# Performance work log

Hardware: AMD Instinct MI355X
Metric: run time of the kernel (lower is better)

Reference implementation:

```python
import jax, jax.numpy as jnp
import numpy as np

ALPHA = 2.0      # spikingjelly surrogate.ATan default alpha
TAU_LIF = 2.0    # LIFNode tau
V_TH = 1.0       # spike threshold (v_reset = 0.0, hard reset)


@jax.custom_vjp
def spike_fn(x):
    # Heaviside forward (spikingjelly: x >= 0 -> 1)
    return (x >= 0.0).astype(x.dtype)

def _spike_fwd(x):
    return spike_fn(x), x

def _spike_bwd(x, g):
    # ATan surrogate gradient: alpha/2 / (1 + (pi/2 * alpha * x)^2)
    return (g * (ALPHA / 2.0) / (1.0 + (jnp.pi / 2.0 * ALPHA * x) ** 2),)

spike_fn.defvjp(_spike_fwd, _spike_bwd)


def setup_inputs() -> dict:
    key = jax.random.key(0)
    ks = jax.random.split(key, 5)
    B, T, I, H, O = 256, 1000, 700, 64, 20
    x = jax.random.normal(ks[0], (B, T, I), dtype=jnp.float32)
    W_h = jax.random.normal(ks[1], (H, I), dtype=jnp.float32) / np.sqrt(I).astype(np.float32)
    b_h = jnp.zeros((H,), dtype=jnp.float32)
    W_r = jax.random.normal(ks[2], (O, H), dtype=jnp.float32) / np.sqrt(H).astype(np.float32)
    b_r = jnp.zeros((O,), dtype=jnp.float32)
    tau_m = jax.random.uniform(ks[3], (O,), dtype=jnp.float32, minval=0.0, maxval=4.0)
    return {"x": x, "W_h": W_h, "b_h": b_h, "W_r": W_r, "b_r": b_r, "tau_m": tau_m}


def reference(x, W_h, b_h, W_r, b_r, tau_m):
    B, T, I = x.shape
    H = W_h.shape[0]
    O = W_r.shape[0]
    # One big GEMM for all hidden input currents: [T, B, H]
    currents = jnp.einsum('bti,hi->tbh', x, W_h) + b_h
    beta = jax.nn.sigmoid(tau_m)  # readout leak [O]
    # original accumulates softmax only for t > 10
    mask = (jnp.arange(T) > 10).astype(x.dtype)

    def step(carry, inp):
        v, v_ro, acc = carry
        cur, m = inp
        # LIF charge (decay_input=True, v_reset=0): v += (cur - v)/tau
        v = v + (cur - v) / TAU_LIF
        s = spike_fn(v - V_TH)
        # hard reset to v_reset = 0
        v = v * (1.0 - s)
        # readout leaky integrator
        ro_in = s @ W_r.T + b_r                      # [B, O]
        v_ro = v_ro * beta + (1.0 - beta) * ro_in
        acc = acc + m * jax.nn.softmax(v_ro, axis=-1)
        return (v, v_ro, acc), None

    init = (jnp.zeros((B, H), x.dtype),
            jnp.zeros((B, O), x.dtype),
            jnp.zeros((B, O), x.dtype))
    (_, _, acc), _ = jax.lax.scan(step, init, (currents, mask))
    return acc
```

## Files before the change

kernel.cpp:

```cpp
#include <hip/hip_runtime.h>


typedef float  f32x4  __attribute__((ext_vector_type(4)));
typedef short  short8 __attribute__((ext_vector_type(8)));
typedef unsigned long long ull;

#define B_   256
#define T_   1000
#define K_   700
#define H_   64
#define O_   20
#define NKT  22
#define TC   10
#define NC   100
#define TCL  100
#define NCL  10
#define BIL  40

#define OFF_WFRAG  ((size_t)0)
#define OFF_CUR    ((size_t)262144)
#define OFF_MASK   ((size_t)65798144)

__global__ void wprep(const float* __restrict__ Wh, unsigned short* __restrict__ wfrag) {
    int e = blockIdx.x * 256 + threadIdx.x;
    int kt   = e >> 8;
    int rem  = e & 255;
    int nf   = rem >> 6;
    int lane = rem & 63;
    int h     = nf * 16 + (lane & 15);
    int kbase = kt * 32 + ((lane >> 4) & 3) * 8;
    unsigned short* dh = wfrag + (size_t)kt * 4096 + (nf * 64 + lane) * 8;
    unsigned short* dl = dh + 2048;
#pragma unroll
    for (int j = 0; j < 8; ++j) {
        int k = kbase + j;
        float v = (k < K_) ? Wh[(size_t)h * K_ + k] : 0.0f;
        unsigned u  = __builtin_bit_cast(unsigned, v);
        float    fh = __builtin_bit_cast(float, u & 0xffff0000u);
        float    r  = v - fh;
        dh[j] = (unsigned short)(u >> 16);
        dl[j] = (unsigned short)(__builtin_bit_cast(unsigned, r) >> 16);
    }
}

__device__ __forceinline__ void glds16(const void* src, void* lds) {
    __builtin_amdgcn_global_load_lds(
        (const __attribute__((address_space(1))) void*)src,
        (__attribute__((address_space(3))) void*)lds, 16, 0, 0);
}

__device__ __forceinline__ void splitpair(f32x4 p0, f32x4 p1, short8& hi, short8& lo) {
#pragma unroll
    for (int j = 0; j < 4; ++j) {
        {
            unsigned u  = __builtin_bit_cast(unsigned, p0[j]);
            float    fh = __builtin_bit_cast(float, u & 0xffff0000u);
            float    r  = p0[j] - fh;
            hi[j] = (short)(u >> 16);
            lo[j] = (short)(__builtin_bit_cast(unsigned, r) >> 16);
        }
        {
            unsigned u  = __builtin_bit_cast(unsigned, p1[j]);
            float    fh = __builtin_bit_cast(float, u & 0xffff0000u);
            float    r  = p1[j] - fh;
            hi[j + 4] = (short)(u >> 16);
            lo[j + 4] = (short)(__builtin_bit_cast(unsigned, r) >> 16);
        }
    }
}

__device__ __forceinline__ void stage_x32(const float* __restrict__ x, size_t row0,
                                          int kt, int lane, int wid, float* sbuf) {
#pragma unroll
    for (int j = 0; j < 4; ++j) {
        int c   = j * 256 + wid * 64 + lane;
        int row = c >> 3;
        int col = c & 7;
        int csw = (col ^ (row & 7)) << 4;
        int kbyte = kt * 128 + csw;
        if (kbyte + 16 > K_ * 4) kbyte = 0;
        const char* src = (const char*)(x + (row0 + row) * (size_t)K_) + kbyte;
        float* dst = sbuf + (size_t)(j * 256 + wid * 64) * 4;
        glds16(src, dst);
    }
}

__device__ __forceinline__ void stage_w32(const unsigned short* __restrict__ wfrag,
                                          int kt, int lane, int wid, unsigned short* sbuf) {
#pragma unroll
    for (int j = 0; j < 2; ++j) {
        int c = j * 256 + wid * 64 + lane;
        int l = c ^ ((c >> 4) & 7);
        const unsigned short* src = wfrag + (size_t)kt * 4096 + l * 8;
        unsigned short* dst = sbuf + (size_t)(j * 256 + wid * 64) * 8;
        glds16(src, dst);
    }
}

__device__ __forceinline__ void compute32(const float* sbx_, const unsigned short* sbw_,
                                          int lane, int wid, f32x4 (&acc)[2][4]) {
    const f32x4*  xb = (const f32x4*)sbx_;
    const short8* wb = (const short8*)sbw_;
    short8 ah[2], al[2];
    int v0 = (lane >> 4) * 2;
#pragma unroll
    for (int i = 0; i < 2; ++i) {
        int r  = wid * 32 + i * 16 + (lane & 15);
        int c0 = r * 8 + (v0 ^ (r & 7));
        int c1 = r * 8 + ((v0 + 1) ^ (r & 7));
        splitpair(xb[c0], xb[c1], ah[i], al[i]);
    }
#pragma unroll
    for (int n = 0; n < 4; ++n) {
        int lh = n * 64 + lane;
        int ph = lh ^ ((lh >> 4) & 7);
        short8 bhf = wb[ph];
        short8 blf = wb[ph + 256];
#pragma unroll
        for (int i = 0; i < 2; ++i) {
            acc[i][n] = __builtin_amdgcn_mfma_f32_16x16x32_bf16(ah[i], bhf, acc[i][n], 0, 0, 0);
            acc[i][n] = __builtin_amdgcn_mfma_f32_16x16x32_bf16(al[i], bhf, acc[i][n], 0, 0, 0);
            acc[i][n] = __builtin_amdgcn_mfma_f32_16x16x32_bf16(ah[i], blf, acc[i][n], 0, 0, 0);
        }
    }
}

__global__ __launch_bounds__(256, 2) void gemm_cur(const float* __restrict__ x,
                                                   const unsigned short* __restrict__ wfrag,
                                                   const float* __restrict__ b_h,
                                                   float* __restrict__ cur) {
    __shared__ float          sbx[3][4096];
    __shared__ unsigned short sbw[3][4096];
    int tid  = threadIdx.x;
    int lane = tid & 63;
    int wid  = tid >> 6;
    size_t row0 = (size_t)blockIdx.x * 128;

    float bh4[4];
#pragma unroll
    for (int n = 0; n < 4; ++n) bh4[n] = b_h[n * 16 + (lane & 15)];

    f32x4 acc[2][4];
#pragma unroll
    for (int i = 0; i < 2; ++i)
#pragma unroll
        for (int n = 0; n < 4; ++n) acc[i][n] = (f32x4){0.f, 0.f, 0.f, 0.f};

    stage_x32(x, row0, 0, lane, wid, sbx[0]);  stage_w32(wfrag, 0, lane, wid, sbw[0]);
    stage_x32(x, row0, 1, lane, wid, sbx[1]);  stage_w32(wfrag, 1, lane, wid, sbw[1]);
    stage_x32(x, row0, 2, lane, wid, sbx[2]);  stage_w32(wfrag, 2, lane, wid, sbw[2]);

#define GSTEP(T, N)                                                          \
    {                                                                        \
        asm volatile("s_waitcnt vmcnt(" #N ")" ::: "memory");                \
        __builtin_amdgcn_s_barrier();                                        \
        compute32(sbx[(T) % 3], sbw[(T) % 3], lane, wid, acc);               \
        asm volatile("s_waitcnt lgkmcnt(0)" ::: "memory");                   \
        __builtin_amdgcn_s_barrier();                                        \
        if ((T) + 3 < NKT) {                                                 \
            stage_x32(x, row0, (T) + 3, lane, wid, sbx[(T) % 3]);            \
            stage_w32(wfrag, (T) + 3, lane, wid, sbw[(T) % 3]);              \
        }                                                                    \
    }
    GSTEP(0, 12)  GSTEP(1, 12)  GSTEP(2, 12)  GSTEP(3, 12)  GSTEP(4, 12)
    GSTEP(5, 12)  GSTEP(6, 12)  GSTEP(7, 12)  GSTEP(8, 12)  GSTEP(9, 12)
    GSTEP(10, 12) GSTEP(11, 12) GSTEP(12, 12) GSTEP(13, 12) GSTEP(14, 12)
    GSTEP(15, 12) GSTEP(16, 12) GSTEP(17, 12) GSTEP(18, 12) GSTEP(19, 12)
    GSTEP(20, 6)  GSTEP(21, 0)
#undef GSTEP

#pragma unroll
    for (int i = 0; i < 2; ++i) {
        size_t row = row0 + wid * 32 + i * 16 + ((lane >> 4) & 3) * 4;
#pragma unroll
        for (int n = 0; n < 4; ++n) {
#pragma unroll
            for (int j = 0; j < 4; ++j) {
                cur[(row + j) * H_ + n * 16 + (lane & 15)] = acc[i][n][j] + bh4[n];
            }
        }
    }
}

__global__ __launch_bounds__(64) void lif(const float* __restrict__ cur, ull* __restrict__ masks) {
    int b = blockIdx.x & 255;
    int c = blockIdx.x >> 8;
    int h = threadIdx.x;
    int t0 = c * TCL;
    int ts = (c == 0) ? 0 : (t0 - BIL);
    const float* p = cur + ((size_t)b * T_ + ts) * H_ + h;
    ull* mp = masks + (size_t)b * T_;
    float v = 0.0f;
#pragma unroll 8
    for (int t = ts; t < t0; ++t) {
        float cc = *p; p += H_;
        v = (v + cc) * 0.5f;
        v = (v >= 1.0f) ? 0.0f : v;
    }
#pragma unroll 8
    for (int t = t0; t < t0 + TCL; ++t) {
        float cc = *p; p += H_;
        v = (v + cc) * 0.5f;
        bool s = (v >= 1.0f);
        ull m = __ballot(s);
        if (h == 0) mp[t] = m;
        v = s ? 0.0f : v;
    }
}

__global__ __launch_bounds__(128) void readout(const ull* __restrict__ masks,
                                               const float* __restrict__ Wr,
                                               const float* __restrict__ br,
                                               const float* __restrict__ tau,
                                               float* __restrict__ out) {
    __shared__ __align__(16) float wt[64][20];
    __shared__ ull  smask[T_];
    __shared__ __align__(16) float E[NC][20];
    __shared__ __align__(16) float Sv[NC][20];
    __shared__ __align__(16) float pacc[NC][20];
    __shared__ __align__(16) float sScale[20], sBase[20], sBeta[20];

    int tid = threadIdx.x;
    int b   = blockIdx.x;
    for (int i = tid; i < 1280; i += 128) wt[i & 63][i >> 6] = Wr[(size_t)(i >> 6) * 64 + (i & 63)];
    for (int i = tid; i < T_; i += 128) smask[i] = masks[(size_t)b * T_ + i];
    if (tid < 20) {
        float beta = 1.0f / (1.0f + __expf(-tau[tid]));
        sBeta[tid]  = beta;
        sScale[tid] = 1.0f - beta;
        sBase[tid]  = br[tid];
    }
    __syncthreads();

    for (int it = tid; it < NC * 5; it += 128) {
        int o4 = it % 5;
        int c  = it / 5;
        f32x4 beta4  = *(const f32x4*)&sBeta[o4 * 4];
        f32x4 scale4 = *(const f32x4*)&sScale[o4 * 4];
        f32x4 base4  = *(const f32x4*)&sBase[o4 * 4];
        f32x4 v = {0.f, 0.f, 0.f, 0.f};
        const ull* mp = smask + c * TC;
        for (int j = 0; j < TC; ++j) {
            ull m = mp[j];
            f32x4 a = {0.f, 0.f, 0.f, 0.f};
            while (m) {
                int h = __builtin_ctzll(m);
                m &= (m - 1);
                a += *(const f32x4*)&wt[h][o4 * 4];
            }
            f32x4 q;
#pragma unroll
            for (int jj = 0; jj < 4; ++jj) q[jj] = scale4[jj] * (base4[jj] + a[jj]);
            v = beta4 * v + q;
        }
        *(f32x4*)&E[c][o4 * 4] = v;
    }
    __syncthreads();

    if (tid < 20) {
        int o = tid;
        float beta = sBeta[o];
        float bp = 1.0f;
#pragma unroll
        for (int i = 0; i < TC; ++i) bp *= beta;
        float s = 0.0f;
        for (int c = 0; c < NC; ++c) {
            Sv[c][o] = s;
            s = bp * s + E[c][o];
        }
    }
    __syncthreads();

    if (tid < NC) {
        int c = tid;
        float beta[20], v[20], acc[20];
#pragma unroll
        for (int o = 0; o < 20; ++o) {
            beta[o] = sBeta[o];
            v[o]   = Sv[c][o];
            acc[o] = 0.0f;
        }
        int t0 = c * TC;
        const ull* mp = smask + t0;
        for (int j = 0; j < TC; ++j) {
            int t = t0 + j;
            ull m = mp[j];
            f32x4 a[5];
#pragma unroll
            for (int i = 0; i < 5; ++i) a[i] = (f32x4){0.f, 0.f, 0.f, 0.f};
            while (m) {
                int h = __builtin_ctzll(m);
                m &= (m - 1);
                const f32x4* w4 = (const f32x4*)&wt[h][0];
#pragma unroll
                for (int i = 0; i < 5; ++i) a[i] += w4[i];
            }
#pragma unroll
            for (int o = 0; o < 20; ++o) {
                float q = sScale[o] * (sBase[o] + a[o >> 2][o & 3]);
                v[o] = beta[o] * v[o] + q;
            }
            if (t >= 11) {
                float mx = v[0];
#pragma unroll
                for (int o = 1; o < 20; ++o) mx = fmaxf(mx, v[o]);
                float e[20], ssum = 0.0f;
#pragma unroll
                for (int o = 0; o < 20; ++o) { e[o] = __expf(v[o] - mx); ssum += e[o]; }
                float inv = 1.0f / ssum;
#pragma unroll
                for (int o = 0; o < 20; ++o) acc[o] += e[o] * inv;
            }
        }
#pragma unroll
        for (int o = 0; o < 20; ++o) pacc[c][o] = acc[o];
    }
    __syncthreads();

    if (tid < 20) {
        float s = 0.0f;
        for (int c = 0; c < NC; ++c) s += pacc[c][tid];
        out[(size_t)b * 20 + tid] = s;
    }
}

extern "C" void kernel_launch(void* const* d_in, const int* in_sizes, int n_in,
                              void* d_out, int out_size, void* d_ws, size_t ws_size,
                              hipStream_t stream) {
    const float* x   = (const float*)d_in[0];
    const float* W_h = (const float*)d_in[1];
    const float* b_h = (const float*)d_in[2];
    const float* W_r = (const float*)d_in[3];
    const float* b_r = (const float*)d_in[4];
    const float* tau = (const float*)d_in[5];

    char* ws = (char*)d_ws;
    unsigned short* wfrag = (unsigned short*)(ws + OFF_WFRAG);
    float* cur  = (float*)(ws + OFF_CUR);
    ull*   msk  = (ull*)(ws + OFF_MASK);
    float* out  = (float*)d_out;

    wprep<<<22, 256, 0, stream>>>(W_h, wfrag);
    gemm_cur<<<2000, 256, 0, stream>>>(x, wfrag, b_h, cur);
    lif<<<NCL * 256, 64, 0, stream>>>(cur, msk);
    readout<<<256, 128, 0, stream>>>(msk, W_r, b_r, tau, out);
}
```

Before: 264.9 us.

## Vectorize current layout, double-buffer GEMM, parallelize readout scan across 512 threads

The GEMM drops from triple to double buffering with occupancy raised to 3 blocks per CU, and it writes currents as float4 groups of four consecutive timesteps per hidden unit. The LIF kernel reads that interleaved layout with vector loads. The readout kernel uses 200 chunks of 5 timesteps with 512 threads, and its serial chunk-prefix scan and final reduction become a two-level hierarchical scan over 8 groups. The aim is to cut load instruction count and serial latency, at the cost of shallower GEMM prefetch and extra barriers in readout.

```diff
diff --git a/kernel.cpp b/kernel.cpp
--- a/kernel.cpp
+++ b/kernel.cpp
@@ -11,8 +11,8 @@
 #define H_   64
 #define O_   20
 #define NKT  22
-#define TC   10
-#define NC   100
+#define NCH  200
+#define TCH  5
 #define TCL  100
 #define NCL  10
 #define BIL  40
@@ -125,12 +125,12 @@
     }
 }
 
-__global__ __launch_bounds__(256, 2) void gemm_cur(const float* __restrict__ x,
+__global__ __launch_bounds__(256, 3) void gemm_cur(const float* __restrict__ x,
                                                    const unsigned short* __restrict__ wfrag,
                                                    const float* __restrict__ b_h,
                                                    float* __restrict__ cur) {
-    __shared__ float          sbx[3][4096];
-    __shared__ unsigned short sbw[3][4096];
+    __shared__ float          sbx[2][4096];
+    __shared__ unsigned short sbw[2][4096];
     int tid  = threadIdx.x;
     int lane = tid & 63;
     int wid  = tid >> 6;
@@ -148,36 +148,36 @@
 
     stage_x32(x, row0, 0, lane, wid, sbx[0]);  stage_w32(wfrag, 0, lane, wid, sbw[0]);
     stage_x32(x, row0, 1, lane, wid, sbx[1]);  stage_w32(wfrag, 1, lane, wid, sbw[1]);
-    stage_x32(x, row0, 2, lane, wid, sbx[2]);  stage_w32(wfrag, 2, lane, wid, sbw[2]);
 
 #define GSTEP(T, N)                                                          \
     {                                                                        \
         asm volatile("s_waitcnt vmcnt(" #N ")" ::: "memory");                \
         __builtin_amdgcn_s_barrier();                                        \
-        compute32(sbx[(T) % 3], sbw[(T) % 3], lane, wid, acc);               \
+        compute32(sbx[(T) & 1], sbw[(T) & 1], lane, wid, acc);               \
         asm volatile("s_waitcnt lgkmcnt(0)" ::: "memory");                   \
         __builtin_amdgcn_s_barrier();                                        \
-        if ((T) + 3 < NKT) {                                                 \
-            stage_x32(x, row0, (T) + 3, lane, wid, sbx[(T) % 3]);            \
-            stage_w32(wfrag, (T) + 3, lane, wid, sbw[(T) % 3]);              \
+        if ((T) + 2 < NKT) {                                                 \
+            stage_x32(x, row0, (T) + 2, lane, wid, sbx[(T) & 1]);            \
+            stage_w32(wfrag, (T) + 2, lane, wid, sbw[(T) & 1]);              \
         }                                                                    \
     }
-    GSTEP(0, 12)  GSTEP(1, 12)  GSTEP(2, 12)  GSTEP(3, 12)  GSTEP(4, 12)
-    GSTEP(5, 12)  GSTEP(6, 12)  GSTEP(7, 12)  GSTEP(8, 12)  GSTEP(9, 12)
-    GSTEP(10, 12) GSTEP(11, 12) GSTEP(12, 12) GSTEP(13, 12) GSTEP(14, 12)
-    GSTEP(15, 12) GSTEP(16, 12) GSTEP(17, 12) GSTEP(18, 12) GSTEP(19, 12)
+    GSTEP(0, 6)   GSTEP(1, 6)   GSTEP(2, 6)   GSTEP(3, 6)   GSTEP(4, 6)
+    GSTEP(5, 6)   GSTEP(6, 6)   GSTEP(7, 6)   GSTEP(8, 6)   GSTEP(9, 6)
+    GSTEP(10, 6)  GSTEP(11, 6)  GSTEP(12, 6)  GSTEP(13, 6)  GSTEP(14, 6)
+    GSTEP(15, 6)  GSTEP(16, 6)  GSTEP(17, 6)  GSTEP(18, 6)  GSTEP(19, 6)
     GSTEP(20, 6)  GSTEP(21, 0)
 #undef GSTEP
 
+    f32x4* cur4 = (f32x4*)cur;
 #pragma unroll
     for (int i = 0; i < 2; ++i) {
-        size_t row = row0 + wid * 32 + i * 16 + ((lane >> 4) & 3) * 4;
+        size_t r4 = row0 + wid * 32 + i * 16 + ((lane >> 4) & 3) * 4;
 #pragma unroll
         for (int n = 0; n < 4; ++n) {
-#pragma unroll
-            for (int j = 0; j < 4; ++j) {
-                cur[(row + j) * H_ + n * 16 + (lane & 15)] = acc[i][n][j] + bh4[n];
-            }
+            f32x4 q;
+#pragma unroll
+            for (int j = 0; j < 4; ++j) q[j] = acc[i][n][j] + bh4[n];
+            cur4[(r4 >> 2) * 64 + n * 16 + (lane & 15)] = q;
         }
     }
 }
@@ -188,42 +188,50 @@
     int h = threadIdx.x;
     int t0 = c * TCL;
     int ts = (c == 0) ? 0 : (t0 - BIL);
-    const float* p = cur + ((size_t)b * T_ + ts) * H_ + h;
-    ull* mp = masks + (size_t)b * T_;
+    const f32x4* p = (const f32x4*)cur + (((size_t)b * T_ + ts) >> 2) * 64 + h;
     float v = 0.0f;
-#pragma unroll 8
-    for (int t = ts; t < t0; ++t) {
-        float cc = *p; p += H_;
-        v = (v + cc) * 0.5f;
-        v = (v >= 1.0f) ? 0.0f : v;
-    }
-#pragma unroll 8
-    for (int t = t0; t < t0 + TCL; ++t) {
-        float cc = *p; p += H_;
-        v = (v + cc) * 0.5f;
-        bool s = (v >= 1.0f);
-        ull m = __ballot(s);
-        if (h == 0) mp[t] = m;
-        v = s ? 0.0f : v;
-    }
-}
-
-__global__ __launch_bounds__(128) void readout(const ull* __restrict__ masks,
+    int ngb = (t0 - ts) >> 2;
+    for (int g = 0; g < ngb; ++g) {
+        f32x4 q = p[g * 64];
+#pragma unroll
+        for (int j = 0; j < 4; ++j) {
+            v = (v + q[j]) * 0.5f;
+            v = (v >= 1.0f) ? 0.0f : v;
+        }
+    }
+    p += (size_t)ngb * 64;
+    ull* mp = masks + (size_t)b * T_ + t0;
+#pragma unroll 2
+    for (int g = 0; g < TCL / 4; ++g) {
+        f32x4 q = p[g * 64];
+#pragma unroll
+        for (int j = 0; j < 4; ++j) {
+            v = (v + q[j]) * 0.5f;
+            bool s = (v >= 1.0f);
+            ull m = __ballot(s);
+            if (h == 0) mp[g * 4 + j] = m;
+            v = s ? 0.0f : v;
+        }
+    }
+}
+
+__global__ __launch_bounds__(512) void readout(const ull* __restrict__ masks,
                                                const float* __restrict__ Wr,
                                                const float* __restrict__ br,
                                                const float* __restrict__ tau,
                                                float* __restrict__ out) {
     __shared__ __align__(16) float wt[64][20];
     __shared__ ull  smask[T_];
-    __shared__ __align__(16) float E[NC][20];
-    __shared__ __align__(16) float Sv[NC][20];
-    __shared__ __align__(16) float pacc[NC][20];
+    __shared__ __align__(16) float E[NCH][20];
+    __shared__ __align__(16) float Sv[NCH][20];
+    __shared__ __align__(16) float pacc[NCH][20];
     __shared__ __align__(16) float sScale[20], sBase[20], sBeta[20];
+    __shared__ float Pg[8][20], Sst[8][20], part[8][20];
 
     int tid = threadIdx.x;
     int b   = blockIdx.x;
-    for (int i = tid; i < 1280; i += 128) wt[i & 63][i >> 6] = Wr[(size_t)(i >> 6) * 64 + (i & 63)];
-    for (int i = tid; i < T_; i += 128) smask[i] = masks[(size_t)b * T_ + i];
+    for (int i = tid; i < 1280; i += 512) wt[i & 63][i >> 6] = Wr[(size_t)(i >> 6) * 64 + (i & 63)];
+    for (int i = tid; i < T_; i += 512) smask[i] = masks[(size_t)b * T_ + i];
     if (tid < 20) {
         float beta = 1.0f / (1.0f + __expf(-tau[tid]));
         sBeta[tid]  = beta;
@@ -232,15 +240,16 @@
     }
     __syncthreads();
 
-    for (int it = tid; it < NC * 5; it += 128) {
+    for (int it = tid; it < NCH * 5; it += 512) {
         int o4 = it % 5;
         int c  = it / 5;
         f32x4 beta4  = *(const f32x4*)&sBeta[o4 * 4];
         f32x4 scale4 = *(const f32x4*)&sScale[o4 * 4];
         f32x4 base4  = *(const f32x4*)&sBase[o4 * 4];
         f32x4 v = {0.f, 0.f, 0.f, 0.f};
-        const ull* mp = smask + c * TC;
-        for (int j = 0; j < TC; ++j) {
+        const ull* mp = smask + c * TCH;
+#pragma unroll
+        for (int j = 0; j < TCH; ++j) {
             ull m = mp[j];
             f32x4 a = {0.f, 0.f, 0.f, 0.f};
             while (m) {
@@ -257,21 +266,41 @@
     }
     __syncthreads();
 
+    if (tid < 160) {
+        int o = tid >> 3, g = tid & 7;
+        float beta = sBeta[o];
+        float b2 = beta * beta;
+        float bp = b2 * b2 * beta;
+        float P = 0.0f;
+        for (int c = g * 25; c < g * 25 + 25; ++c) P = bp * P + E[c][o];
+        Pg[g][o] = P;
+    }
+    __syncthreads();
+
     if (tid < 20) {
         int o = tid;
         float beta = sBeta[o];
-        float bp = 1.0f;
-#pragma unroll
-        for (int i = 0; i < TC; ++i) bp *= beta;
+        float b2 = beta * beta;
+        float bp = b2 * b2 * beta;
+        float bp25 = 1.0f;
+#pragma unroll
+        for (int i = 0; i < 25; ++i) bp25 *= bp;
         float s = 0.0f;
-        for (int c = 0; c < NC; ++c) {
-            Sv[c][o] = s;
-            s = bp * s + E[c][o];
-        }
-    }
-    __syncthreads();
-
-    if (tid < NC) {
+        for (int g = 0; g < 8; ++g) { Sst[g][o] = s; s = bp25 * s + Pg[g][o]; }
+    }
+    __syncthreads();
+
+    if (tid < 160) {
+        int o = tid >> 3, g = tid & 7;
+        float beta = sBeta[o];
+        float b2 = beta * beta;
+        float bp = b2 * b2 * beta;
+        float s = Sst[g][o];
+        for (int c = g * 25; c < g * 25 + 25; ++c) { Sv[c][o] = s; s = bp * s + E[c][o]; }
+    }
+    __syncthreads();
+
+    if (tid < NCH) {
         int c = tid;
         float beta[20], v[20], acc[20];
 #pragma unroll
@@ -280,9 +309,10 @@
             v[o]   = Sv[c][o];
             acc[o] = 0.0f;
         }
-        int t0 = c * TC;
+        int t0 = c * TCH;
         const ull* mp = smask + t0;
-        for (int j = 0; j < TC; ++j) {
+#pragma unroll
+        for (int j = 0; j < TCH; ++j) {
             int t = t0 + j;
             ull m = mp[j];
             f32x4 a[5];
@@ -317,9 +347,17 @@
     }
     __syncthreads();
 
+    if (tid < 160) {
+        int o = tid >> 3, g = tid & 7;
+        float s = 0.0f;
+        for (int c = g * 25; c < g * 25 + 25; ++c) s += pacc[c][o];
+        part[g][o] = s;
+    }
+    __syncthreads();
     if (tid < 20) {
         float s = 0.0f;
-        for (int c = 0; c < NC; ++c) s += pacc[c][tid];
+#pragma unroll
+        for (int g = 0; g < 8; ++g) s += part[g][tid];
         out[(size_t)b * 20 + tid] = s;
     }
 }
@@ -343,5 +381,5 @@
     wprep<<<22, 256, 0, stream>>>(W_h, wfrag);
     gemm_cur<<<2000, 256, 0, stream>>>(x, wfrag, b_h, cur);
     lif<<<NCL * 256, 64, 0, stream>>>(cur, msk);
-    readout<<<256, 128, 0, stream>>>(msk, W_r, b_r, tau, out);
-}
+    readout<<<256, 512, 0, stream>>>(msk, W_r, b_r, tau, out);
+}
```

Measured after the change: 218.3 us. -17.6%, faster.
